# Kernel optimization log

Hardware: AMD Instinct MI355X
Metric: run time of the kernel (lower is better)

The kernel has to match this reference:

```python
import jax, jax.numpy as jnp
import numpy as np

VOCAB = 32000
EMB = 256
HID = 512
PAD = 0
INIT = 1
MAX_LEN = 64
BATCH = 64


def setup_inputs() -> dict:
    key = jax.random.key(0)
    ks = jax.random.split(key, 12)
    rng = np.random.RandomState(0)
    # token ids with end-padding (pack_padded_sequence semantics): lengths in [T/2, T]
    lengths = rng.randint(MAX_LEN // 2, MAX_LEN + 1, size=(BATCH,))
    toks = rng.randint(2, VOCAB, size=(BATCH, MAX_LEN))
    mask = np.arange(MAX_LEN)[None, :] < lengths[:, None]
    toks = np.where(mask, toks, PAD)
    inputs = jnp.asarray(toks, dtype=jnp.int64) if jax.config.jax_enable_x64 else jnp.asarray(toks, dtype=jnp.int32)
    s = 0.05
    return {
        "inputs": inputs,
        "emb": jax.random.normal(ks[0], (VOCAB, EMB), jnp.float32) * s,
        "enc_Wih": jax.random.normal(ks[1], (4 * HID, EMB), jnp.float32) * s,
        "enc_Whh": jax.random.normal(ks[2], (4 * HID, HID), jnp.float32) * s,
        "enc_bih": jax.random.normal(ks[3], (4 * HID,), jnp.float32) * s,
        "enc_bhh": jax.random.normal(ks[4], (4 * HID,), jnp.float32) * s,
        "dec_Wih": jax.random.normal(ks[5], (4 * HID, EMB), jnp.float32) * s,
        "dec_Whh": jax.random.normal(ks[6], (4 * HID, HID), jnp.float32) * s,
        "dec_bih": jax.random.normal(ks[7], (4 * HID,), jnp.float32) * s,
        "dec_bhh": jax.random.normal(ks[8], (4 * HID,), jnp.float32) * s,
        "lin_W": jax.random.normal(ks[9], (VOCAB, HID), jnp.float32) * s,
        "lin_b": jax.random.normal(ks[10], (VOCAB,), jnp.float32) * s,
    }


def _lstm_cell(x, h, c, Wih, Whh, bih, bhh):
    # PyTorch gate order: i, f, g, o
    gates = x @ Wih.T + bih + h @ Whh.T + bhh  # [B, 4H]
    i, f, g, o = jnp.split(gates, 4, axis=-1)
    c_new = jax.nn.sigmoid(f) * c + jax.nn.sigmoid(i) * jnp.tanh(g)
    h_new = jax.nn.sigmoid(o) * jnp.tanh(c_new)
    return h_new, c_new


def reference(inputs, emb, enc_Wih, enc_Whh, enc_bih, enc_bhh,
              dec_Wih, dec_Whh, dec_bih, dec_bhh, lin_W, lin_b):
    B, T = inputs.shape
    lengths = jnp.sum(inputs != PAD, axis=1)  # [B]
    # ---- encoder: masked LSTM scan; final h equals packed-sequence last hidden ----
    x_emb = jnp.transpose(emb[inputs], (1, 0, 2))  # [T, B, E]
    step_mask = (jnp.arange(T)[:, None] < lengths[None, :])[..., None]  # [T, B, 1]

    def enc_step(carry, xs):
        h, c = carry
        xt, m = xs
        h_new, c_new = _lstm_cell(xt, h, c, enc_Wih, enc_Whh, enc_bih, enc_bhh)
        h = jnp.where(m, h_new, h)
        c = jnp.where(m, c_new, c)
        return (h, c), None

    h0 = jnp.zeros((B, HID), x_emb.dtype)
    (z, _), _ = jax.lax.scan(enc_step, (h0, h0), (x_emb, step_mask))

    # ---- decoder: teacher forcing with targets = inputs ----
    init_tok = jnp.full((B, 1), INIT, dtype=inputs.dtype)
    dec_idx = jnp.concatenate([init_tok, inputs[:, :-1]], axis=1)  # [B, T]
    dec_emb = jnp.transpose(emb[dec_idx], (1, 0, 2))  # [T, B, E]

    def dec_step(carry, xt):
        h, c = carry
        h, c = _lstm_cell(xt, h, c, dec_Wih, dec_Whh, dec_bih, dec_bhh)
        return (h, c), h

    c0 = jnp.zeros((B, HID), z.dtype)
    _, hs = jax.lax.scan(dec_step, (z, c0), dec_emb)  # hs: [T, B, H]

    logits = jnp.einsum('tbh,vh->btv', hs, lin_W) + lin_b  # [B, T, V]
    return logits
```

## Files before the change

### kernel.cpp

```cpp
#include <hip/hip_runtime.h>
#include <math.h>

#define ST 64
#define NBAT 64
#define ED 256
#define HD 512
#define G4 2048
#define VO 32000
#define NWORK 64
#define NLOG 192
#define NTILES (VO / 128)
#define SLOT32 (NBAT * HD / 2)

typedef unsigned int u32;
typedef __bf16 bf16;
typedef bf16 bf16x8 __attribute__((ext_vector_type(8)));
typedef float f32x4 __attribute__((ext_vector_type(4)));

__device__ __forceinline__ float sigm(float x) { return 1.f / (1.f + expf(-x)); }


__global__ void k_lengths(const int* __restrict__ toks, int* __restrict__ len) {
  int b = threadIdx.x;
  if (b < NBAT) {
    int n = 0;
    for (int t = 0; t < ST; ++t) n += (toks[b * ST + t] != 0) ? 1 : 0;
    len[b] = n;
  }
}

#define SEG0 (G4 * ED)
#define SEG1 (SEG0 + G4 * HD)
#define SEG2 (SEG1 + G4 * ED)
#define SEG3 (SEG2 + G4 * HD)
#define SEG4 (SEG3 + G4)
#define SEG5 (SEG4 + G4)
__global__ void k_prep(const float* __restrict__ eWih, const float* __restrict__ eWhh,
                       const float* __restrict__ dWih, const float* __restrict__ dWhh,
                       const float* __restrict__ ebih, const float* __restrict__ ebhh,
                       const float* __restrict__ dbih, const float* __restrict__ dbhh,
                       bf16* __restrict__ WihEb, bf16* __restrict__ WhhEb,
                       bf16* __restrict__ WihDb, bf16* __restrict__ WhhDb,
                       float* __restrict__ bsumE, float* __restrict__ bsumD) {
  int i = blockIdx.x * blockDim.x + threadIdx.x;
  if (i < SEG0)      WihEb[i] = (bf16)eWih[i];
  else if (i < SEG1) WhhEb[i - SEG0] = (bf16)eWhh[i - SEG0];
  else if (i < SEG2) WihDb[i - SEG1] = (bf16)dWih[i - SEG1];
  else if (i < SEG3) WhhDb[i - SEG2] = (bf16)dWhh[i - SEG2];
  else if (i < SEG4) { int j = i - SEG3; bsumE[j] = ebih[j] + ebhh[j]; }
  else if (i < SEG5) { int j = i - SEG4; bsumD[j] = dbih[j] + dbhh[j]; }
}

__global__ void k_gather(const int* __restrict__ toks, const float* __restrict__ emb,
                         bf16* __restrict__ encX, bf16* __restrict__ decX) {
  int i = blockIdx.x * blockDim.x + threadIdx.x;
  if (i >= ST * NBAT * ED) return;
  int e = i % ED;
  int tb = i / ED;
  int b = tb % NBAT;
  int t = tb / NBAT;
  int te = toks[b * ST + t];
  encX[i] = (bf16)emb[te * ED + e];
  int td = (t == 0) ? 1 : toks[b * ST + t - 1];
  decX[i] = (bf16)emb[td * ED + e];
}

__global__ __launch_bounds__(512, 2) void k_fused(
    const bf16* __restrict__ encX, const bf16* __restrict__ decX,
    const bf16* __restrict__ WihE, const bf16* __restrict__ WhhE,
    const bf16* __restrict__ WihD, const bf16* __restrict__ WhhD,
    const float* __restrict__ bsumE, const float* __restrict__ bsumD,
    const int* __restrict__ len,
    const float* __restrict__ linW, const float* __restrict__ linb,
    float* __restrict__ out,
    u32* __restrict__ hx32,
    u32* flags,
    u32* decgo)
{
  __shared__ __align__(16) char smem[133632];

  const int tid  = threadIdx.x;
  const int lane = tid & 63;
  const int wid  = tid >> 6;
  const int blk  = blockIdx.x;
  const int r16  = lane & 15;
  const int kh   = lane >> 4;
  const int kc   = kh * 8;

  if (blk < NWORK) {
    auto Wr  = (bf16(*)[HD + 8])smem;
    auto Wx  = (bf16(*)[ED + 8])(smem + 33280);
    auto gl  = (float(*)[64][33])(smem + 50176);
    u32* go_lds = (u32*)(smem + 67072);
    u32* dcnt   = (u32*)(smem + 67076);

    const int wm   = wid & 3;
    const int wn   = wid >> 2;
    const int u0   = blk * 8;
    const int hi   = kh;
    const int arow = 16 * wm + r16;
    const int brow = 16 * wn + r16;

    const int eb   = (tid & 255) >> 2;
    const int j2   = (tid & 3) * 2;
    const int elen = len[eb];

    if (tid == 0) { *go_lds = 0; *dcnt = 0; }
    u32 hp = 0;

    for (int phase = 0; phase < 2; ++phase) {
      const bf16* Wih  = phase ? WihD : WihE;
      const bf16* Whh  = phase ? WhhD : WhhE;
      const float* bsum = phase ? bsumD : bsumE;
      const bf16* Xall = phase ? decX : encX;

      for (int idx = tid; idx < 32 * HD; idx += 512) {
        int n = idx >> 9, k = idx & (HD - 1);
        Wr[n][k] = Whh[((n >> 3) * HD + u0 + (n & 7)) * HD + k];
      }
      for (int idx = tid; idx < 32 * ED; idx += 512) {
        int n = idx >> 8, k = idx & (ED - 1);
        Wx[n][k] = Wih[((n >> 3) * HD + u0 + (n & 7)) * ED + k];
      }
      const float bi0 = bsum[0 * HD + u0 + j2], bi1 = bsum[0 * HD + u0 + j2 + 1];
      const float bf0 = bsum[1 * HD + u0 + j2], bf1 = bsum[1 * HD + u0 + j2 + 1];
      const float bg0 = bsum[2 * HD + u0 + j2], bg1 = bsum[2 * HD + u0 + j2 + 1];
      const float bo0 = bsum[3 * HD + u0 + j2], bo1 = bsum[3 * HD + u0 + j2 + 1];
      float c0 = 0.f, c1 = 0.f;
      __syncthreads();

      for (int t = 0; t < ST; ++t) {
        const int step = phase * ST + t;
        const int par  = step & 1;
        u32* hxout = hx32 + (size_t)(step + 1) * SLOT32 + blk * 256;
        const bf16* xin = Xall + t * (NBAT * ED);

        f32x4 acc1 = {0.f, 0.f, 0.f, 0.f};
        #pragma unroll
        for (int kk = 0; kk < ED / 32; ++kk) {
          bf16x8 av = *(const bf16x8*)(xin + arow * ED + kk * 32 + kc);
          bf16x8 bv = *(const bf16x8*)(&Wx[brow][kk * 32 + kc]);
          acc1 = __builtin_amdgcn_mfma_f32_16x16x32_bf16(av, bv, acc1, 0, 0, 0);
        }

        if (step > 0) {
          if (wid == 0) {
            u32 f = __hip_atomic_load(&flags[lane], __ATOMIC_RELAXED,
                                      __HIP_MEMORY_SCOPE_AGENT);
            while (!__all((int)(f >= (u32)step))) {
              __builtin_amdgcn_s_sleep(1);
              f = __hip_atomic_load(&flags[lane], __ATOMIC_RELAXED,
                                    __HIP_MEMORY_SCOPE_AGENT);
            }
            if (lane == 0) {
              __hip_atomic_store(go_lds, (u32)step, __ATOMIC_RELAXED,
                                 __HIP_MEMORY_SCOPE_WORKGROUP);
              if (blk == 0)
                __hip_atomic_store(decgo, (u32)step, __ATOMIC_RELAXED,
                                   __HIP_MEMORY_SCOPE_AGENT);
            }
          } else {
            u32 g = __hip_atomic_load(go_lds, __ATOMIC_RELAXED,
                                      __HIP_MEMORY_SCOPE_WORKGROUP);
            while (g < (u32)step) {
              __builtin_amdgcn_s_sleep(1);
              g = __hip_atomic_load(go_lds, __ATOMIC_RELAXED,
                                    __HIP_MEMORY_SCOPE_WORKGROUP);
            }
          }
          __builtin_amdgcn_fence(__ATOMIC_ACQUIRE, "wavefront");
          __builtin_amdgcn_sched_barrier(0);
        }

        const bf16* hbase = (const bf16*)(hx32 + (size_t)step * SLOT32);
        const bf16* hptr  = hbase + (size_t)hi * 512 + arow * 8;
        f32x4 accA = {0.f, 0.f, 0.f, 0.f};
        f32x4 accB = {0.f, 0.f, 0.f, 0.f};
        #pragma unroll
        for (int kk = 0; kk < 16; kk += 2) {
          bf16x8 a0 = *(const bf16x8*)(hptr + (size_t)kk * 2048);
          bf16x8 a1 = *(const bf16x8*)(hptr + (size_t)(kk + 1) * 2048);
          bf16x8 b0 = *(const bf16x8*)(&Wr[brow][kk * 32 + kc]);
          bf16x8 b1 = *(const bf16x8*)(&Wr[brow][(kk + 1) * 32 + kc]);
          accA = __builtin_amdgcn_mfma_f32_16x16x32_bf16(a0, b0, accA, 0, 0, 0);
          accB = __builtin_amdgcn_mfma_f32_16x16x32_bf16(a1, b1, accB, 0, 0, 0);
        }
        #pragma unroll
        for (int r = 0; r < 4; ++r)
          gl[par][16 * wm + kh * 4 + r][16 * wn + r16] = accA[r] + accB[r] + acc1[r];
        __syncthreads();

        if (tid < 256) {
          float gi0 = gl[par][eb][j2]      + bi0, gi1 = gl[par][eb][j2 + 1]  + bi1;
          float gf0 = gl[par][eb][8 + j2]  + bf0, gf1 = gl[par][eb][9 + j2]  + bf1;
          float gg0 = gl[par][eb][16 + j2] + bg0, gg1 = gl[par][eb][17 + j2] + bg1;
          float go0 = gl[par][eb][24 + j2] + bo0, go1 = gl[par][eb][25 + j2] + bo1;
          bool upd = (phase == 1) || (t < elen);
          float cn0 = sigm(gf0) * c0 + sigm(gi0) * tanhf(gg0);
          float cn1 = sigm(gf1) * c1 + sigm(gi1) * tanhf(gg1);
          float hn0 = sigm(go0) * tanhf(cn0);
          float hn1 = sigm(go1) * tanhf(cn1);
          if (upd) {
            c0 = cn0; c1 = cn1;
            union { u32 u; bf16 h[2]; } pk;
            pk.h[0] = (bf16)hn0; pk.h[1] = (bf16)hn1;
            hp = pk.u;
          }
          __hip_atomic_store(&hxout[tid], hp, __ATOMIC_RELAXED,
                             __HIP_MEMORY_SCOPE_AGENT);
          asm volatile("s_waitcnt vmcnt(0)" ::: "memory");
          __builtin_amdgcn_sched_barrier(0);
          if (lane == 0)
            __hip_atomic_fetch_add(dcnt, 1u, __ATOMIC_RELAXED,
                                   __HIP_MEMORY_SCOPE_WORKGROUP);
          if (wid == 3) {
            u32 c = __hip_atomic_load(dcnt, __ATOMIC_RELAXED,
                                      __HIP_MEMORY_SCOPE_WORKGROUP);
            while (c < 4u * (u32)(step + 1)) {
              __builtin_amdgcn_s_sleep(1);
              c = __hip_atomic_load(dcnt, __ATOMIC_RELAXED,
                                    __HIP_MEMORY_SCOPE_WORKGROUP);
            }
            if (lane == 0)
              __hip_atomic_store(&flags[blk], (u32)(step + 1), __ATOMIC_RELAXED,
                                 __HIP_MEMORY_SCOPE_AGENT);
          }
        }
      }
    }

    if (blk == 0 && wid == 0) {
      u32 f = __hip_atomic_load(&flags[lane], __ATOMIC_RELAXED,
                                __HIP_MEMORY_SCOPE_AGENT);
      while (!__all((int)(f >= (u32)(2 * ST)))) {
        __builtin_amdgcn_s_sleep(1);
        f = __hip_atomic_load(&flags[lane], __ATOMIC_RELAXED,
                              __HIP_MEMORY_SCOPE_AGENT);
      }
      if (lane == 0)
        __hip_atomic_store(decgo, (u32)(2 * ST), __ATOMIC_RELAXED,
                           __HIP_MEMORY_SCOPE_AGENT);
    }
  } else {
    auto Bs = (bf16(*)[HD + 8])smem;
    u32* bgo = (u32*)(smem + 133120);
    const int lid = blk - NWORK;
    const int wm = wid & 3, wn = wid >> 2;
    const int arow = 16 * wm + r16;

    if (tid == 0) *bgo = 0;

    for (int nt = lid; nt < NTILES; nt += NLOG) {
      __syncthreads();
      for (int idx = tid; idx < 128 * (HD / 8); idx += 512) {
        int n = idx >> 6, k8 = (idx & 63) * 8;
        const float* bsrc = linW + (size_t)(nt * 128 + n) * HD + k8;
        f32x4 x0 = *(const f32x4*)bsrc;
        f32x4 x1 = *(const f32x4*)(bsrc + 4);
        bf16x8 bv;
        #pragma unroll
        for (int e = 0; e < 4; ++e) { bv[e] = (bf16)x0[e]; bv[4 + e] = (bf16)x1[e]; }
        *(bf16x8*)&Bs[n][k8] = bv;
      }
      __syncthreads();

      for (int t = 0; t < ST; ++t) {
        const u32 target = (u32)(ST + 1 + t);
        if (wid == 0) {
          u32 v = __hip_atomic_load(decgo, __ATOMIC_RELAXED,
                                    __HIP_MEMORY_SCOPE_AGENT);
          while (v < target) {
            __builtin_amdgcn_s_sleep(64);
            v = __hip_atomic_load(decgo, __ATOMIC_RELAXED,
                                  __HIP_MEMORY_SCOPE_AGENT);
          }
          if (lane == 0)
            __hip_atomic_store(bgo, v, __ATOMIC_RELAXED,
                               __HIP_MEMORY_SCOPE_WORKGROUP);
        } else {
          u32 g = __hip_atomic_load(bgo, __ATOMIC_RELAXED,
                                    __HIP_MEMORY_SCOPE_WORKGROUP);
          while (g < target) {
            __builtin_amdgcn_s_sleep(8);
            g = __hip_atomic_load(bgo, __ATOMIC_RELAXED,
                                  __HIP_MEMORY_SCOPE_WORKGROUP);
          }
        }
        __builtin_amdgcn_fence(__ATOMIC_ACQUIRE, "wavefront");
        __builtin_amdgcn_sched_barrier(0);

        const bf16* slotA = (const bf16*)(hx32 + (size_t)target * SLOT32);
        const bf16* aptr  = slotA + (size_t)kh * 512 + arow * 8;
        f32x4 acc[4];
        #pragma unroll
        for (int jj = 0; jj < 4; ++jj) acc[jj] = (f32x4){0.f, 0.f, 0.f, 0.f};
        #pragma unroll
        for (int kk = 0; kk < 16; ++kk) {
          int kks = (kk + lid) & 15;
          bf16x8 av = *(const bf16x8*)(aptr + (size_t)kks * 2048);
          #pragma unroll
          for (int jj = 0; jj < 4; ++jj) {
            bf16x8 bv = *(const bf16x8*)(&Bs[64 * wn + 16 * jj + r16][kks * 32 + kc]);
            acc[jj] = __builtin_amdgcn_mfma_f32_16x16x32_bf16(av, bv, acc[jj], 0, 0, 0);
          }
        }
        #pragma unroll
        for (int jj = 0; jj < 4; ++jj) {
          int col = nt * 128 + 64 * wn + 16 * jj + r16;
          float bias = linb[col];
          #pragma unroll
          for (int r = 0; r < 4; ++r) {
            int b = 16 * wm + kh * 4 + r;
            out[((size_t)b * ST + t) * VO + col] = acc[jj][r] + bias;
          }
        }
      }
    }
  }
}


extern "C" void kernel_launch(void* const* d_in, const int* in_sizes, int n_in,
                              void* d_out, int out_size, void* d_ws, size_t ws_size,
                              hipStream_t stream) {
  const int*   toks = (const int*)d_in[0];
  const float* emb  = (const float*)d_in[1];
  const float* eWih = (const float*)d_in[2];
  const float* eWhh = (const float*)d_in[3];
  const float* ebih = (const float*)d_in[4];
  const float* ebhh = (const float*)d_in[5];
  const float* dWih = (const float*)d_in[6];
  const float* dWhh = (const float*)d_in[7];
  const float* dbih = (const float*)d_in[8];
  const float* dbhh = (const float*)d_in[9];
  const float* linW = (const float*)d_in[10];
  const float* linb = (const float*)d_in[11];
  float* out = (float*)d_out;

  char* ws = (char*)d_ws;
  size_t off = 0;
  auto alloc = [&](size_t bytes) {
    void* p = ws + off;
    off = (off + bytes + 255) & ~(size_t)255;
    return p;
  };
  bf16* encX  = (bf16*)alloc((size_t)ST * NBAT * ED * 2);
  bf16* decX  = (bf16*)alloc((size_t)ST * NBAT * ED * 2);
  bf16* WihEb = (bf16*)alloc((size_t)G4 * ED * 2);
  bf16* WhhEb = (bf16*)alloc((size_t)G4 * HD * 2);
  bf16* WihDb = (bf16*)alloc((size_t)G4 * ED * 2);
  bf16* WhhDb = (bf16*)alloc((size_t)G4 * HD * 2);
  float* bsumE = (float*)alloc(G4 * 4);
  float* bsumD = (float*)alloc(G4 * 4);
  u32*  hx    = (u32*)alloc((size_t)(2 * ST + 1) * SLOT32 * 4);
  int*  len   = (int*)alloc(NBAT * 4);
  u32*  flags = (u32*)alloc(4096);
  u32*  decgo = flags + 64;

  hipMemsetAsync(hx, 0, (size_t)SLOT32 * 4, stream);
  hipMemsetAsync(flags, 0, 4096, stream);

  k_lengths<<<1, 64, 0, stream>>>(toks, len);
  k_prep<<<(SEG5 + 255) / 256, 256, 0, stream>>>(
      eWih, eWhh, dWih, dWhh, ebih, ebhh, dbih, dbhh,
      WihEb, WhhEb, WihDb, WhhDb, bsumE, bsumD);
  k_gather<<<(ST * NBAT * ED + 255) / 256, 256, 0, stream>>>(toks, emb, encX, decX);

  k_fused<<<NWORK + NLOG, 512, 0, stream>>>(
      encX, decX, WihEb, WhhEb, WihDb, WhhDb, bsumE, bsumD, len,
      linW, linb, out, hx, flags, decgo);
}
```

Before: 752.3 us.

## Add dedicated poller wave with per-chunk readiness mask and rebalance logits tiles

```diff
diff --git a/kernel.cpp b/kernel.cpp
--- a/kernel.cpp
+++ b/kernel.cpp
@@ -11,8 +11,10 @@
 #define NLOG 192
 #define NTILES (VO / 128)
 #define SLOT32 (NBAT * HD / 2)
+#define NTHR 576
 
 typedef unsigned int u32;
+typedef unsigned long long u64;
 typedef __bf16 bf16;
 typedef bf16 bf16x8 __attribute__((ext_vector_type(8)));
 typedef float f32x4 __attribute__((ext_vector_type(4)));
@@ -65,7 +67,7 @@
   decX[i] = (bf16)emb[td * ED + e];
 }
 
-__global__ __launch_bounds__(512, 2) void k_fused(
+__global__ __launch_bounds__(NTHR, 1) void k_fused(
     const bf16* __restrict__ encX, const bf16* __restrict__ decX,
     const bf16* __restrict__ WihE, const bf16* __restrict__ WhhE,
     const bf16* __restrict__ WihD, const bf16* __restrict__ WhhD,
@@ -91,11 +93,11 @@
     auto Wr  = (bf16(*)[HD + 8])smem;
     auto Wx  = (bf16(*)[ED + 8])(smem + 33280);
     auto gl  = (float(*)[64][33])(smem + 50176);
-    u32* go_lds = (u32*)(smem + 67072);
-    u32* dcnt   = (u32*)(smem + 67076);
+    u32* gmask = (u32*)(smem + 67072);
+    u32* dcnt  = (u32*)(smem + 67080);
 
     const int wm   = wid & 3;
-    const int wn   = wid >> 2;
+    const int wn   = (wid >> 2) & 1;
     const int u0   = blk * 8;
     const int hi   = kh;
     const int arow = 16 * wm + r16;
@@ -105,7 +107,7 @@
     const int j2   = (tid & 3) * 2;
     const int elen = len[eb];
 
-    if (tid == 0) { *go_lds = 0; *dcnt = 0; }
+    if (tid == 0) { gmask[0] = 0; gmask[1] = 0; *dcnt = 0; }
     u32 hp = 0;
 
     for (int phase = 0; phase < 2; ++phase) {
@@ -114,11 +116,11 @@
       const float* bsum = phase ? bsumD : bsumE;
       const bf16* Xall = phase ? decX : encX;
 
-      for (int idx = tid; idx < 32 * HD; idx += 512) {
+      for (int idx = tid; idx < 32 * HD; idx += NTHR) {
         int n = idx >> 9, k = idx & (HD - 1);
         Wr[n][k] = Whh[((n >> 3) * HD + u0 + (n & 7)) * HD + k];
       }
-      for (int idx = tid; idx < 32 * ED; idx += 512) {
+      for (int idx = tid; idx < 32 * ED; idx += NTHR) {
         int n = idx >> 8, k = idx & (ED - 1);
         Wx[n][k] = Wih[((n >> 3) * HD + u0 + (n & 7)) * ED + k];
       }
@@ -132,104 +134,112 @@
       for (int t = 0; t < ST; ++t) {
         const int step = phase * ST + t;
         const int par  = step & 1;
-        u32* hxout = hx32 + (size_t)(step + 1) * SLOT32 + blk * 256;
-        const bf16* xin = Xall + t * (NBAT * ED);
-
-        f32x4 acc1 = {0.f, 0.f, 0.f, 0.f};
-        #pragma unroll
-        for (int kk = 0; kk < ED / 32; ++kk) {
-          bf16x8 av = *(const bf16x8*)(xin + arow * ED + kk * 32 + kc);
-          bf16x8 bv = *(const bf16x8*)(&Wx[brow][kk * 32 + kc]);
-          acc1 = __builtin_amdgcn_mfma_f32_16x16x32_bf16(av, bv, acc1, 0, 0, 0);
-        }
-
-        if (step > 0) {
-          if (wid == 0) {
-            u32 f = __hip_atomic_load(&flags[lane], __ATOMIC_RELAXED,
-                                      __HIP_MEMORY_SCOPE_AGENT);
-            while (!__all((int)(f >= (u32)step))) {
+
+        if (wid == 8) {
+          if (lane == 0)
+            __hip_atomic_store(&gmask[par ^ 1], 0u, __ATOMIC_RELAXED,
+                               __HIP_MEMORY_SCOPE_WORKGROUP);
+          if (step > 0) {
+            for (;;) {
+              u32 f = __hip_atomic_load(&flags[lane], __ATOMIC_RELAXED,
+                                        __HIP_MEMORY_SCOPE_AGENT);
+              u64 bal = __ballot((int)(f >= (u32)step));
+              u32 m = 0;
+              #pragma unroll
+              for (int g = 0; g < 16; ++g)
+                if (((bal >> (4 * g)) & 0xFull) == 0xFull) m |= (1u << g);
+              if (lane == 0)
+                __hip_atomic_store(&gmask[par], m, __ATOMIC_RELAXED,
+                                   __HIP_MEMORY_SCOPE_WORKGROUP);
+              if (bal == ~0ull) break;
               __builtin_amdgcn_s_sleep(1);
-              f = __hip_atomic_load(&flags[lane], __ATOMIC_RELAXED,
-                                    __HIP_MEMORY_SCOPE_AGENT);
             }
-            if (lane == 0) {
-              __hip_atomic_store(go_lds, (u32)step, __ATOMIC_RELAXED,
-                                 __HIP_MEMORY_SCOPE_WORKGROUP);
-              if (blk == 0)
-                __hip_atomic_store(decgo, (u32)step, __ATOMIC_RELAXED,
+            if (blk == 0 && lane == 0)
+              __hip_atomic_store(decgo, (u32)step, __ATOMIC_RELAXED,
+                                 __HIP_MEMORY_SCOPE_AGENT);
+          }
+          __syncthreads();
+        } else {
+          u32* hxout = hx32 + (size_t)(step + 1) * SLOT32 + blk * 256;
+          const bf16* xin = Xall + t * (NBAT * ED);
+
+          f32x4 acc1 = {0.f, 0.f, 0.f, 0.f};
+          #pragma unroll
+          for (int kk = 0; kk < ED / 32; ++kk) {
+            bf16x8 av = *(const bf16x8*)(xin + arow * ED + kk * 32 + kc);
+            bf16x8 bv = *(const bf16x8*)(&Wx[brow][kk * 32 + kc]);
+            acc1 = __builtin_amdgcn_mfma_f32_16x16x32_bf16(av, bv, acc1, 0, 0, 0);
+          }
+
+          const bf16* hbase = (const bf16*)(hx32 + (size_t)step * SLOT32);
+          const bf16* hptr  = hbase + (size_t)hi * 512 + arow * 8;
+          f32x4 accA = {0.f, 0.f, 0.f, 0.f};
+          f32x4 accB = {0.f, 0.f, 0.f, 0.f};
+          #pragma unroll
+          for (int kkx = 0; kkx < 16; ++kkx) {
+            int kk = (kkx + 2 * wid) & 15;
+            if (step > 0) {
+              u32 m = __hip_atomic_load(&gmask[par], __ATOMIC_RELAXED,
+                                        __HIP_MEMORY_SCOPE_WORKGROUP);
+              while (!((m >> kk) & 1u)) {
+                __builtin_amdgcn_s_sleep(1);
+                m = __hip_atomic_load(&gmask[par], __ATOMIC_RELAXED,
+                                      __HIP_MEMORY_SCOPE_WORKGROUP);
+              }
+              __builtin_amdgcn_fence(__ATOMIC_ACQUIRE, "wavefront");
+              __builtin_amdgcn_sched_barrier(0);
+            }
+            bf16x8 a = *(const bf16x8*)(hptr + (size_t)kk * 2048);
+            bf16x8 b = *(const bf16x8*)(&Wr[brow][kk * 32 + kc]);
+            if (kkx & 1) accB = __builtin_amdgcn_mfma_f32_16x16x32_bf16(a, b, accB, 0, 0, 0);
+            else         accA = __builtin_amdgcn_mfma_f32_16x16x32_bf16(a, b, accA, 0, 0, 0);
+          }
+          #pragma unroll
+          for (int r = 0; r < 4; ++r)
+            gl[par][16 * wm + kh * 4 + r][16 * wn + r16] = accA[r] + accB[r] + acc1[r];
+          __syncthreads();
+
+          if (tid < 256) {
+            float gi0 = gl[par][eb][j2]      + bi0, gi1 = gl[par][eb][j2 + 1]  + bi1;
+            float gf0 = gl[par][eb][8 + j2]  + bf0, gf1 = gl[par][eb][9 + j2]  + bf1;
+            float gg0 = gl[par][eb][16 + j2] + bg0, gg1 = gl[par][eb][17 + j2] + bg1;
+            float go0 = gl[par][eb][24 + j2] + bo0, go1 = gl[par][eb][25 + j2] + bo1;
+            bool upd = (phase == 1) || (t < elen);
+            float cn0 = sigm(gf0) * c0 + sigm(gi0) * tanhf(gg0);
+            float cn1 = sigm(gf1) * c1 + sigm(gi1) * tanhf(gg1);
+            float hn0 = sigm(go0) * tanhf(cn0);
+            float hn1 = sigm(go1) * tanhf(cn1);
+            if (upd) {
+              c0 = cn0; c1 = cn1;
+              union { u32 u; bf16 h[2]; } pk;
+              pk.h[0] = (bf16)hn0; pk.h[1] = (bf16)hn1;
+              hp = pk.u;
+            }
+            __hip_atomic_store(&hxout[tid], hp, __ATOMIC_RELAXED,
+                               __HIP_MEMORY_SCOPE_AGENT);
+            asm volatile("s_waitcnt vmcnt(0)" ::: "memory");
+            __builtin_amdgcn_sched_barrier(0);
+            if (lane == 0)
+              __hip_atomic_fetch_add(dcnt, 1u, __ATOMIC_RELAXED,
+                                     __HIP_MEMORY_SCOPE_WORKGROUP);
+            if (wid == 3) {
+              u32 c = __hip_atomic_load(dcnt, __ATOMIC_RELAXED,
+                                        __HIP_MEMORY_SCOPE_WORKGROUP);
+              while (c < 4u * (u32)(step + 1)) {
+                __builtin_amdgcn_s_sleep(1);
+                c = __hip_atomic_load(dcnt, __ATOMIC_RELAXED,
+                                      __HIP_MEMORY_SCOPE_WORKGROUP);
+              }
+              if (lane == 0)
+                __hip_atomic_store(&flags[blk], (u32)(step + 1), __ATOMIC_RELAXED,
                                    __HIP_MEMORY_SCOPE_AGENT);
             }
-          } else {
-            u32 g = __hip_atomic_load(go_lds, __ATOMIC_RELAXED,
-                                      __HIP_MEMORY_SCOPE_WORKGROUP);
-            while (g < (u32)step) {
-              __builtin_amdgcn_s_sleep(1);
-              g = __hip_atomic_load(go_lds, __ATOMIC_RELAXED,
-                                    __HIP_MEMORY_SCOPE_WORKGROUP);
-            }
-          }
-          __builtin_amdgcn_fence(__ATOMIC_ACQUIRE, "wavefront");
-          __builtin_amdgcn_sched_barrier(0);
+          }
         }
-
-        const bf16* hbase = (const bf16*)(hx32 + (size_t)step * SLOT32);
-        const bf16* hptr  = hbase + (size_t)hi * 512 + arow * 8;
-        f32x4 accA = {0.f, 0.f, 0.f, 0.f};
-        f32x4 accB = {0.f, 0.f, 0.f, 0.f};
-        #pragma unroll
-        for (int kk = 0; kk < 16; kk += 2) {
-          bf16x8 a0 = *(const bf16x8*)(hptr + (size_t)kk * 2048);
-          bf16x8 a1 = *(const bf16x8*)(hptr + (size_t)(kk + 1) * 2048);
-          bf16x8 b0 = *(const bf16x8*)(&Wr[brow][kk * 32 + kc]);
-          bf16x8 b1 = *(const bf16x8*)(&Wr[brow][(kk + 1) * 32 + kc]);
-          accA = __builtin_amdgcn_mfma_f32_16x16x32_bf16(a0, b0, accA, 0, 0, 0);
-          accB = __builtin_amdgcn_mfma_f32_16x16x32_bf16(a1, b1, accB, 0, 0, 0);
-        }
-        #pragma unroll
-        for (int r = 0; r < 4; ++r)
-          gl[par][16 * wm + kh * 4 + r][16 * wn + r16] = accA[r] + accB[r] + acc1[r];
-        __syncthreads();
-
-        if (tid < 256) {
-          float gi0 = gl[par][eb][j2]      + bi0, gi1 = gl[par][eb][j2 + 1]  + bi1;
-          float gf0 = gl[par][eb][8 + j2]  + bf0, gf1 = gl[par][eb][9 + j2]  + bf1;
-          float gg0 = gl[par][eb][16 + j2] + bg0, gg1 = gl[par][eb][17 + j2] + bg1;
-          float go0 = gl[par][eb][24 + j2] + bo0, go1 = gl[par][eb][25 + j2] + bo1;
-          bool upd = (phase == 1) || (t < elen);
-          float cn0 = sigm(gf0) * c0 + sigm(gi0) * tanhf(gg0);
-          float cn1 = sigm(gf1) * c1 + sigm(gi1) * tanhf(gg1);
-          float hn0 = sigm(go0) * tanhf(cn0);
-          float hn1 = sigm(go1) * tanhf(cn1);
-          if (upd) {
-            c0 = cn0; c1 = cn1;
-            union { u32 u; bf16 h[2]; } pk;
-            pk.h[0] = (bf16)hn0; pk.h[1] = (bf16)hn1;
-            hp = pk.u;
-          }
-          __hip_atomic_store(&hxout[tid], hp, __ATOMIC_RELAXED,
-                             __HIP_MEMORY_SCOPE_AGENT);
-          asm volatile("s_waitcnt vmcnt(0)" ::: "memory");
-          __builtin_amdgcn_sched_barrier(0);
-          if (lane == 0)
-            __hip_atomic_fetch_add(dcnt, 1u, __ATOMIC_RELAXED,
-                                   __HIP_MEMORY_SCOPE_WORKGROUP);
-          if (wid == 3) {
-            u32 c = __hip_atomic_load(dcnt, __ATOMIC_RELAXED,
-                                      __HIP_MEMORY_SCOPE_WORKGROUP);
-            while (c < 4u * (u32)(step + 1)) {
-              __builtin_amdgcn_s_sleep(1);
-              c = __hip_atomic_load(dcnt, __ATOMIC_RELAXED,
-                                    __HIP_MEMORY_SCOPE_WORKGROUP);
-            }
-            if (lane == 0)
-              __hip_atomic_store(&flags[blk], (u32)(step + 1), __ATOMIC_RELAXED,
-                                 __HIP_MEMORY_SCOPE_AGENT);
-          }
-        }
       }
     }
 
-    if (blk == 0 && wid == 0) {
+    if (blk == 0 && wid == 8) {
       u32 f = __hip_atomic_load(&flags[lane], __ATOMIC_RELAXED,
                                 __HIP_MEMORY_SCOPE_AGENT);
       while (!__all((int)(f >= (u32)(2 * ST)))) {
@@ -245,14 +255,14 @@
     auto Bs = (bf16(*)[HD + 8])smem;
     u32* bgo = (u32*)(smem + 133120);
     const int lid = blk - NWORK;
-    const int wm = wid & 3, wn = wid >> 2;
+    const int wm = wid & 3, wn = (wid >> 2) & 1;
     const int arow = 16 * wm + r16;
 
     if (tid == 0) *bgo = 0;
 
-    for (int nt = lid; nt < NTILES; nt += NLOG) {
+    auto run_tile = [&](int nt, int tlo, int thi) {
       __syncthreads();
-      for (int idx = tid; idx < 128 * (HD / 8); idx += 512) {
+      for (int idx = tid; idx < 128 * (HD / 8); idx += NTHR) {
         int n = idx >> 6, k8 = (idx & 63) * 8;
         const float* bsrc = linW + (size_t)(nt * 128 + n) * HD + k8;
         f32x4 x0 = *(const f32x4*)bsrc;
@@ -263,8 +273,9 @@
         *(bf16x8*)&Bs[n][k8] = bv;
       }
       __syncthreads();
-
-      for (int t = 0; t < ST; ++t) {
+      if (wid >= 8) return;
+
+      for (int t = tlo; t < thi; ++t) {
         const u32 target = (u32)(ST + 1 + t);
         if (wid == 0) {
           u32 v = __hip_atomic_load(decgo, __ATOMIC_RELAXED,
@@ -315,6 +326,16 @@
           }
         }
       }
+    };
+
+    if (lid < 116) {
+      run_tile(192 + lid / 2, (lid & 1) * 22, (lid & 1) * 22 + 22);
+      run_tile(lid, 0, ST);
+    } else if (lid < 174) {
+      run_tile(lid, 0, ST);
+      run_tile(192 + (lid - 116), 44, ST);
+    } else {
+      run_tile(lid, 0, ST);
     }
   }
 }
@@ -366,7 +387,7 @@
       WihEb, WhhEb, WihDb, WhhDb, bsumE, bsumD);
   k_gather<<<(ST * NBAT * ED + 255) / 256, 256, 0, stream>>>(toks, emb, encX, decX);
 
-  k_fused<<<NWORK + NLOG, 512, 0, stream>>>(
+  k_fused<<<NWORK + NLOG, NTHR, 0, stream>>>(
       encX, decX, WihEb, WhhEb, WihDb, WhhDb, bsumE, bsumD, len,
       linW, linb, out, hx, flags, decgo);
 }
```

Result: slower. 1.027 ms (+36.5%).
